# Kernel optimization log

Measured on AMD Instinct MI355X. Metric: run time of the kernel, lower is better.

The kernel has to match this reference:

```python
import jax, jax.numpy as jnp
import numpy as np

B, N, ATTR, H, OUT, STEPS = 8, 4096, 16, 64, 1, 8


def setup_inputs() -> dict:
    key = jax.random.key(0)
    ks = jax.random.split(key, 12)
    attr_matrix = jax.random.normal(ks[0], (B, N, ATTR), jnp.float32)
    adj_matrix = (jax.random.uniform(ks[1], (B, N, N)) < 0.01).astype(jnp.float32)
    s = float(1.0 / np.sqrt(H))
    u = lambda k, shape: jax.random.uniform(k, shape, jnp.float32, -s, s)
    Wi = jax.random.normal(ks[2], (H, ATTR), jnp.float32) * float(np.sqrt(2.0 / ATTR))  # kaiming
    bi = jnp.zeros((H,), jnp.float32)
    Wz = u(ks[3], (H, 3 * H)); bz = u(ks[4], (H,))
    Wr = u(ks[5], (H, 3 * H)); br = u(ks[6], (H,))
    Wh = u(ks[7], (H, 3 * H)); bh = u(ks[8], (H,))
    Wo = jax.random.normal(ks[9], (OUT, H), jnp.float32) * float(np.sqrt(2.0 / (H + OUT)))  # xavier
    bo = jnp.zeros((OUT,), jnp.float32)
    return dict(attr_matrix=attr_matrix, adj_matrix=adj_matrix, Wi=Wi, bi=bi,
                Wz=Wz, bz=bz, Wr=Wr, br=br, Wh=Wh, bh=bh, Wo=Wo, bo=bo)


def reference(attr_matrix, adj_matrix, Wi, bi, Wz, bz, Wr, br, Wh, bh, Wo, bo):
    # initial node states: (B, N, H)
    h = jax.nn.relu(attr_matrix @ Wi.T + bi)
    A_in = adj_matrix
    A_out = jnp.swapaxes(adj_matrix, -1, -2)
    for _ in range(STEPS):
        a_in = jnp.einsum('bij,bjh->bih', A_in, h)
        a_out = jnp.einsum('bij,bjh->bih', A_out, h)
        inp = jnp.concatenate([a_in, a_out], axis=-1)           # (B, N, 2H)
        xs = jnp.concatenate([inp, h], axis=-1)                  # (B, N, 3H)
        z = jax.nn.sigmoid(xs @ Wz.T + bz)
        r = jax.nn.sigmoid(xs @ Wr.T + br)
        hn = jnp.tanh(jnp.concatenate([inp, r * h], axis=-1) @ Wh.T + bh)
        h = (1.0 - z) * h + z * hn
    return h @ Wo.T + bo  # (B, N, OUT)
```

## Files before the change

kernel.cpp:

```cpp
#include <hip/hip_runtime.h>
#include <hip/hip_fp16.h>
#include <stdint.h>

#define BB 8
#define NN 4096
#define ATTRD 16
#define HD 64
#define STEPS 8
#define NODES (BB*NN)
#define ECAP 96
#define KPAD 196

typedef _Float16 half8 __attribute__((ext_vector_type(8)));
typedef float floatx4 __attribute__((ext_vector_type(4)));
typedef unsigned long long ull;

__global__ void init_h_kernel(const float* __restrict__ attr, const float* __restrict__ Wi,
                              const float* __restrict__ bi, float* __restrict__ h,
                              __half* __restrict__ h16) {
    int idx = blockIdx.x * blockDim.x + threadIdx.x;
    if (idx >= (NODES + 1) * HD) return;
    if (idx >= NODES * HD) {
        h16[idx] = __float2half(0.f);
        return;
    }
    int node = idx >> 6, l = idx & 63;
    const float* a = attr + node * ATTRD;
    const float* w = Wi + l * ATTRD;
    float acc = bi[l];
#pragma unroll
    for (int k = 0; k < ATTRD; k++) acc += a[k] * w[k];
    float r = acc > 0.f ? acc : 0.f;
    h[idx] = r;
    h16[idx] = __float2half(r);
}

__global__ void wprep_kernel(const float* __restrict__ Wz, const float* __restrict__ Wr,
                             const float* __restrict__ Wh,
                             _Float16* __restrict__ wf_hi, _Float16* __restrict__ wf_lo) {
    int t = blockIdx.x * blockDim.x + threadIdx.x;
    if (t >= 3 * 4 * 6 * 64 * 8) return;
    int mat = t / 12288, rem = t % 12288;
    int tile = rem / 3072, rem2 = rem % 3072;
    int kc = rem2 / 512, rem3 = rem2 % 512;
    int lane = rem3 / 8, j = rem3 % 8;
    int k = kc * 32 + (lane >> 4) * 8 + j;
    int och = tile * 16 + (lane & 15);
    const float* W = (mat == 0) ? Wz : (mat == 1) ? Wr : Wh;
    float v = W[och * 192 + k];
    _Float16 hi = (_Float16)v;
    wf_hi[t] = hi;
    wf_lo[t] = (_Float16)(v - (float)hi);
}

__global__ __launch_bounds__(256) void count_rows_kernel(const float4* __restrict__ A4,
                                                         int* __restrict__ cnt_in,
                                                         int* __restrict__ edge_in,
                                                         int* __restrict__ cnt_out,
                                                         int* __restrict__ edge_out) {
    int wave = threadIdx.x >> 6, l = threadIdx.x & 63;
    int row = blockIdx.x * 4 + wave;
    const float4* rp = A4 + (size_t)row * 1024;
    ull mask_lt = (l == 63) ? ~0ull >> 1 : ((1ull << (l + 1)) - 1) >> 1;
    float4 v[16];
#pragma unroll
    for (int t = 0; t < 16; t++) v[t] = rp[t * 64 + l];
    int colbase = (row >> 12) << 12;
    int run = 0;
    int* erow = edge_in + row * ECAP;
#pragma unroll
    for (int t = 0; t < 16; t++) {
        ull b0 = __ballot(v[t].x != 0.f);
        ull b1 = __ballot(v[t].y != 0.f);
        ull b2 = __ballot(v[t].z != 0.f);
        ull b3 = __ballot(v[t].w != 0.f);
        int pre = __popcll(b0 & mask_lt) + __popcll(b1 & mask_lt) +
                  __popcll(b2 & mask_lt) + __popcll(b3 & mask_lt);
        float vv[4] = {v[t].x, v[t].y, v[t].z, v[t].w};
        int jbase = (t * 64 + l) * 4;
        int inner = 0;
#pragma unroll
        for (int q = 0; q < 4; q++) {
            if (vv[q] != 0.f) {
                int col = colbase | (jbase + q);
                int slot = run + pre + inner;
                if (slot < ECAP) erow[slot] = col;
                inner++;
                int s2 = atomicAdd(&cnt_out[col], 1);
                if (s2 < ECAP) edge_out[col * ECAP + s2] = row;
            }
        }
        run += __popcll(b0) + __popcll(b1) + __popcll(b2) + __popcll(b3);
    }
    if (l == 0) cnt_in[row] = run;
}

__global__ __launch_bounds__(256) void aggregate_kernel(
        const uint4* __restrict__ h4, const float* __restrict__ h,
        const int* __restrict__ cnt_in, const int* __restrict__ edge_in,
        const int* __restrict__ cnt_out, const int* __restrict__ edge_out,
        float* __restrict__ xs) {
    int bid = blockIdx.x;
    int batch = bid & 7;
    int group = bid >> 3;
    int wave = threadIdx.x >> 6;
    int node = (batch << 12) + group * 4 + wave;
    int l = threadIdx.x & 63;
    int sub = l >> 3;
    int part = l & 7;
    int ni = cnt_in[node];  if (ni > ECAP) ni = ECAP;
    int no = cnt_out[node]; if (no > ECAP) no = ECAP;
    const int* ei = edge_in + node * ECAP;
    const int* eo = edge_out + node * ECAP;
    int ei0 = ei[l], ei1 = ei[64 + (l & 31)];
    int eo0 = eo[l], eo1 = eo[64 + (l & 31)];
    float ai[8] = {0.f, 0.f, 0.f, 0.f, 0.f, 0.f, 0.f, 0.f};
    float ao[8] = {0.f, 0.f, 0.f, 0.f, 0.f, 0.f, 0.f, 0.f};
    int nmax = ni > no ? ni : no;
    for (int s = 0; s < nmax; s += 32) {
        uint4 gA[4], gB[4];
#pragma unroll
        for (int k = 0; k < 4; k++) {
            int il = s + k * 8 + sub;
            int gi = (il < 64) ? __shfl(ei0, il) : __shfl(ei1, il - 64);
            int go = (il < 64) ? __shfl(eo0, il) : __shfl(eo1, il - 64);
            gi = (il < ni) ? gi : NODES;
            go = (il < no) ? go : NODES;
            gA[k] = h4[(gi << 3) | part];
            gB[k] = h4[(go << 3) | part];
        }
        const __half2* hA0 = (const __half2*)&gA[0];
        const __half2* hA1 = (const __half2*)&gA[1];
        const __half2* hA2 = (const __half2*)&gA[2];
        const __half2* hA3 = (const __half2*)&gA[3];
        const __half2* hB0 = (const __half2*)&gB[0];
        const __half2* hB1 = (const __half2*)&gB[1];
        const __half2* hB2 = (const __half2*)&gB[2];
        const __half2* hB3 = (const __half2*)&gB[3];
#pragma unroll
        for (int k = 0; k < 4; k++) {
            __half2 sA = __hadd2(__hadd2(hA0[k], hA1[k]), __hadd2(hA2[k], hA3[k]));
            __half2 sB = __hadd2(__hadd2(hB0[k], hB1[k]), __hadd2(hB2[k], hB3[k]));
            float2 fA = __half22float2(sA);
            float2 fB = __half22float2(sB);
            ai[2 * k] += fA.x; ai[2 * k + 1] += fA.y;
            ao[2 * k] += fB.x; ao[2 * k + 1] += fB.y;
        }
    }
#pragma unroll
    for (int off = 8; off < 64; off <<= 1) {
#pragma unroll
        for (int k = 0; k < 8; k++) {
            ai[k] += __shfl_xor(ai[k], off);
            ao[k] += __shfl_xor(ao[k], off);
        }
    }
    if (l < 8) {
        float* dst = xs + node * 192;
        float4 si0 = {ai[0], ai[1], ai[2], ai[3]};
        float4 si1 = {ai[4], ai[5], ai[6], ai[7]};
        float4 so0 = {ao[0], ao[1], ao[2], ao[3]};
        float4 so1 = {ao[4], ao[5], ao[6], ao[7]};
        *(float4*)(dst + l * 8)          = si0;
        *(float4*)(dst + l * 8 + 4)      = si1;
        *(float4*)(dst + 64 + l * 8)     = so0;
        *(float4*)(dst + 64 + l * 8 + 4) = so1;
    }
    xs[node * 192 + 128 + l] = h[(node << 6) | l];
}

__global__ __launch_bounds__(256) void gate_kernel(
        const float* __restrict__ xs_g,
        const _Float16* __restrict__ wf_hi, const _Float16* __restrict__ wf_lo,
        const float* __restrict__ bz, const float* __restrict__ br,
        const float* __restrict__ bh,
        float* __restrict__ h, __half* __restrict__ h16) {
    __shared__ float xs_t[16][KPAD];
    int bid = blockIdx.x;
    int base = ((bid & 7) << 12) | ((bid >> 3) << 4);
    int tid = threadIdx.x;
    {
        const float4* src = (const float4*)(xs_g + base * 192);
#pragma unroll
        for (int i = 0; i < 3; i++) {
            int idx = tid + i * 256;
            float4 v = src[idx];
            int nl = idx / 48, kb = (idx % 48) * 4;
            *(float4*)&xs_t[nl][kb] = v;
        }
    }
    __syncthreads();
    int wave = tid >> 6, lane = tid & 63;
    int m = lane & 15, q = lane >> 4;
    int ch = wave * 16 + m;
    const half8* WH = (const half8*)wf_hi;
    const half8* WL = (const half8*)wf_lo;

    floatx4 accz = {0.f, 0.f, 0.f, 0.f};
    floatx4 accr = {0.f, 0.f, 0.f, 0.f};
#pragma unroll
    for (int kc = 0; kc < 6; kc++) {
        const float* xr = &xs_t[m][kc * 32 + q * 8];
        float4 xa = *(const float4*)xr;
        float4 xb = *(const float4*)(xr + 4);
        float xv[8] = {xa.x, xa.y, xa.z, xa.w, xb.x, xb.y, xb.z, xb.w};
        half8 ahi, alo;
#pragma unroll
        for (int j = 0; j < 8; j++) {
            _Float16 hj = (_Float16)xv[j];
            ahi[j] = hj;
            alo[j] = (_Float16)(xv[j] - (float)hj);
        }
        half8 bzh = WH[((0 * 4 + wave) * 6 + kc) * 64 + lane];
        half8 bzl = WL[((0 * 4 + wave) * 6 + kc) * 64 + lane];
        half8 brh = WH[((1 * 4 + wave) * 6 + kc) * 64 + lane];
        half8 brl = WL[((1 * 4 + wave) * 6 + kc) * 64 + lane];
        accz = __builtin_amdgcn_mfma_f32_16x16x32_f16(ahi, bzh, accz, 0, 0, 0);
        accz = __builtin_amdgcn_mfma_f32_16x16x32_f16(alo, bzh, accz, 0, 0, 0);
        accz = __builtin_amdgcn_mfma_f32_16x16x32_f16(ahi, bzl, accz, 0, 0, 0);
        accr = __builtin_amdgcn_mfma_f32_16x16x32_f16(ahi, brh, accr, 0, 0, 0);
        accr = __builtin_amdgcn_mfma_f32_16x16x32_f16(alo, brh, accr, 0, 0, 0);
        accr = __builtin_amdgcn_mfma_f32_16x16x32_f16(ahi, brl, accr, 0, 0, 0);
    }
    float bzv = bz[ch], brv = br[ch], bhv = bh[ch];
    float zreg[4], hvreg[4], rh[4];
#pragma unroll
    for (int rg = 0; rg < 4; rg++) {
        int nl = q * 4 + rg;
        float z = 1.f / (1.f + __expf(-(accz[rg] + bzv)));
        float r = 1.f / (1.f + __expf(-(accr[rg] + brv)));
        float hv = xs_t[nl][128 + ch];
        zreg[rg] = z; hvreg[rg] = hv; rh[rg] = r * hv;
    }
    __syncthreads();
#pragma unroll
    for (int rg = 0; rg < 4; rg++) xs_t[q * 4 + rg][128 + ch] = rh[rg];
    __syncthreads();

    floatx4 acch = {0.f, 0.f, 0.f, 0.f};
#pragma unroll
    for (int kc = 0; kc < 6; kc++) {
        const float* xr = &xs_t[m][kc * 32 + q * 8];
        float4 xa = *(const float4*)xr;
        float4 xb = *(const float4*)(xr + 4);
        float xv[8] = {xa.x, xa.y, xa.z, xa.w, xb.x, xb.y, xb.z, xb.w};
        half8 ahi, alo;
#pragma unroll
        for (int j = 0; j < 8; j++) {
            _Float16 hj = (_Float16)xv[j];
            ahi[j] = hj;
            alo[j] = (_Float16)(xv[j] - (float)hj);
        }
        half8 bhh = WH[((2 * 4 + wave) * 6 + kc) * 64 + lane];
        half8 bhl = WL[((2 * 4 + wave) * 6 + kc) * 64 + lane];
        acch = __builtin_amdgcn_mfma_f32_16x16x32_f16(ahi, bhh, acch, 0, 0, 0);
        acch = __builtin_amdgcn_mfma_f32_16x16x32_f16(alo, bhh, acch, 0, 0, 0);
        acch = __builtin_amdgcn_mfma_f32_16x16x32_f16(ahi, bhl, acch, 0, 0, 0);
    }
    __syncthreads();
#pragma unroll
    for (int rg = 0; rg < 4; rg++) {
        int nl = q * 4 + rg;
        float pre = acch[rg] + bhv;
        float th = 2.f / (1.f + __expf(-2.f * pre)) - 1.f;
        float hv = hvreg[rg];
        xs_t[nl][ch] = hv + zreg[rg] * (th - hv);
    }
    __syncthreads();
    {
        int f = tid * 4;
        int nl = f >> 6, c = f & 63;
        float4 v = *(const float4*)&xs_t[nl][c];
        int gi = ((base + nl) << 6) | c;
        *(float4*)&h[gi] = v;
        __half2 p0 = {__float2half(v.x), __float2half(v.y)};
        __half2 p1 = {__float2half(v.z), __float2half(v.w)};
        *(__half2*)&h16[gi] = p0;
        *(__half2*)&h16[gi + 2] = p1;
    }
}

__global__ void out_kernel(const float* __restrict__ h, const float* __restrict__ Wo,
                           const float* __restrict__ bo, float* __restrict__ out) {
    int wid = (blockIdx.x * blockDim.x + threadIdx.x) >> 6;
    int l = threadIdx.x & 63;
    if (wid >= NODES) return;
    float p = h[(wid << 6) | l] * Wo[l];
#pragma unroll
    for (int off = 32; off > 0; off >>= 1) p += __shfl_down(p, off);
    if (l == 0) out[wid] = p + bo[0];
}

extern "C" void kernel_launch(void* const* d_in, const int* in_sizes, int n_in,
                              void* d_out, int out_size, void* d_ws, size_t ws_size,
                              hipStream_t stream) {
    const float* attr = (const float*)d_in[0];
    const float* adj  = (const float*)d_in[1];
    const float* Wi   = (const float*)d_in[2];
    const float* bi   = (const float*)d_in[3];
    const float* Wz   = (const float*)d_in[4];
    const float* bz   = (const float*)d_in[5];
    const float* Wr   = (const float*)d_in[6];
    const float* br   = (const float*)d_in[7];
    const float* Wh   = (const float*)d_in[8];
    const float* bh   = (const float*)d_in[9];
    const float* Wo   = (const float*)d_in[10];
    const float* bo   = (const float*)d_in[11];
    float* out = (float*)d_out;

    char* ws = (char*)d_ws;
    size_t off = 0;
    auto carve = [&](size_t bytes) { void* p = ws + off; off = (off + bytes + 255) & ~(size_t)255; return p; };
    float* h      = (float*)carve((size_t)NODES * HD * 4);
    __half* h16   = (__half*)carve((size_t)(NODES + 1) * HD * 2);
    float* xs     = (float*)carve((size_t)NODES * 192 * 4);
    _Float16* wf_hi = (_Float16*)carve(3 * 4 * 6 * 64 * 8 * 2);
    _Float16* wf_lo = (_Float16*)carve(3 * 4 * 6 * 64 * 8 * 2);
    int* cnt_in   = (int*)carve((size_t)NODES * 4);
    int* cnt_out  = (int*)carve((size_t)NODES * 4);
    int* edge_in  = (int*)carve((size_t)NODES * ECAP * 4);
    int* edge_out = (int*)carve((size_t)NODES * ECAP * 4);

    hipMemsetAsync(cnt_out, 0, (size_t)NODES * 4, stream);

    init_h_kernel<<<((NODES + 1) * HD + 255) / 256, 256, 0, stream>>>(attr, Wi, bi, h, h16);
    wprep_kernel<<<(3 * 4 * 6 * 64 * 8 + 255) / 256, 256, 0, stream>>>(Wz, Wr, Wh, wf_hi, wf_lo);
    count_rows_kernel<<<NODES / 4, 256, 0, stream>>>((const float4*)adj, cnt_in, edge_in,
                                                     cnt_out, edge_out);

    for (int step = 0; step < STEPS; ++step) {
        aggregate_kernel<<<NODES / 4, 256, 0, stream>>>(
            (const uint4*)h16, h, cnt_in, edge_in, cnt_out, edge_out, xs);
        gate_kernel<<<NODES / 16, 256, 0, stream>>>(xs, wf_hi, wf_lo, bz, br, bh, h, h16);
    }
    out_kernel<<<NODES * HD / 256, 256, 0, stream>>>(h, Wo, bo, out);
}
```

Baseline: 1.185 ms.

## Fuse aggregation and GRU gate into one step kernel with ping-pong h buffers

Merges the per-step aggregate and gate kernels into a single kernel that keeps the 192-wide concatenated input for 4 nodes in shared memory rather than writing and rereading an xs buffer in global memory. Because blocks now read neighbours' h while other blocks write the new state, h and its fp16 copy are double-buffered and swapped each step. The cost is that each block handles only 4 nodes, so the 16-row MFMA tiles are 3/4 redundant (rows are replicated via m&3), and weight loads are repeated by four times as many blocks.

```diff
diff --git a/kernel.cpp b/kernel.cpp
--- a/kernel.cpp
+++ b/kernel.cpp
@@ -17,11 +17,12 @@
 
 __global__ void init_h_kernel(const float* __restrict__ attr, const float* __restrict__ Wi,
                               const float* __restrict__ bi, float* __restrict__ h,
-                              __half* __restrict__ h16) {
+                              __half* __restrict__ h16a, __half* __restrict__ h16b) {
     int idx = blockIdx.x * blockDim.x + threadIdx.x;
     if (idx >= (NODES + 1) * HD) return;
     if (idx >= NODES * HD) {
-        h16[idx] = __float2half(0.f);
+        h16a[idx] = __float2half(0.f);
+        h16b[idx] = __float2half(0.f);
         return;
     }
     int node = idx >> 6, l = idx & 63;
@@ -32,7 +33,7 @@
     for (int k = 0; k < ATTRD; k++) acc += a[k] * w[k];
     float r = acc > 0.f ? acc : 0.f;
     h[idx] = r;
-    h16[idx] = __float2half(r);
+    h16a[idx] = __float2half(r);
 }
 
 __global__ void wprep_kernel(const float* __restrict__ Wz, const float* __restrict__ Wr,
@@ -95,17 +96,32 @@
     if (l == 0) cnt_in[row] = run;
 }
 
-__global__ __launch_bounds__(256) void aggregate_kernel(
-        const uint4* __restrict__ h4, const float* __restrict__ h,
+__global__ __launch_bounds__(256) void step_kernel(
+        const uint4* __restrict__ h4, const float* __restrict__ hg,
         const int* __restrict__ cnt_in, const int* __restrict__ edge_in,
         const int* __restrict__ cnt_out, const int* __restrict__ edge_out,
-        float* __restrict__ xs) {
+        const _Float16* __restrict__ wf_hi, const _Float16* __restrict__ wf_lo,
+        const float* __restrict__ bz, const float* __restrict__ br,
+        const float* __restrict__ bh,
+        float* __restrict__ h_out, __half* __restrict__ h16_out) {
+    __shared__ float xs_t[4][KPAD];
+    __shared__ float h32s[4][64];
+
     int bid = blockIdx.x;
     int batch = bid & 7;
     int group = bid >> 3;
-    int wave = threadIdx.x >> 6;
-    int node = (batch << 12) + group * 4 + wave;
-    int l = threadIdx.x & 63;
+    int node_base = (batch << 12) + group * 4;
+    int tid = threadIdx.x;
+    int wave = tid >> 6, l = tid & 63;
+
+    {
+        int nl = tid >> 6, c = tid & 63;
+        float v = hg[((node_base + nl) << 6) | c];
+        h32s[nl][c] = v;
+        xs_t[nl][128 + c] = v;
+    }
+
+    int node = node_base + wave;
     int sub = l >> 3;
     int part = l & 7;
     int ni = cnt_in[node];  if (ni > ECAP) ni = ECAP;
@@ -156,7 +172,7 @@
         }
     }
     if (l < 8) {
-        float* dst = xs + node * 192;
+        float* dst = &xs_t[wave][0];
         float4 si0 = {ai[0], ai[1], ai[2], ai[3]};
         float4 si1 = {ai[4], ai[5], ai[6], ai[7]};
         float4 so0 = {ao[0], ao[1], ao[2], ao[3]};
@@ -166,32 +182,10 @@
         *(float4*)(dst + 64 + l * 8)     = so0;
         *(float4*)(dst + 64 + l * 8 + 4) = so1;
     }
-    xs[node * 192 + 128 + l] = h[(node << 6) | l];
-}
-
-__global__ __launch_bounds__(256) void gate_kernel(
-        const float* __restrict__ xs_g,
-        const _Float16* __restrict__ wf_hi, const _Float16* __restrict__ wf_lo,
-        const float* __restrict__ bz, const float* __restrict__ br,
-        const float* __restrict__ bh,
-        float* __restrict__ h, __half* __restrict__ h16) {
-    __shared__ float xs_t[16][KPAD];
-    int bid = blockIdx.x;
-    int base = ((bid & 7) << 12) | ((bid >> 3) << 4);
-    int tid = threadIdx.x;
-    {
-        const float4* src = (const float4*)(xs_g + base * 192);
-#pragma unroll
-        for (int i = 0; i < 3; i++) {
-            int idx = tid + i * 256;
-            float4 v = src[idx];
-            int nl = idx / 48, kb = (idx % 48) * 4;
-            *(float4*)&xs_t[nl][kb] = v;
-        }
-    }
-    __syncthreads();
-    int wave = tid >> 6, lane = tid & 63;
-    int m = lane & 15, q = lane >> 4;
+    __syncthreads();
+
+    int m = l & 15, q = l >> 4;
+    int mm = m & 3;
     int ch = wave * 16 + m;
     const half8* WH = (const half8*)wf_hi;
     const half8* WL = (const half8*)wf_lo;
@@ -200,7 +194,7 @@
     floatx4 accr = {0.f, 0.f, 0.f, 0.f};
 #pragma unroll
     for (int kc = 0; kc < 6; kc++) {
-        const float* xr = &xs_t[m][kc * 32 + q * 8];
+        const float* xr = &xs_t[mm][kc * 32 + q * 8];
         float4 xa = *(const float4*)xr;
         float4 xb = *(const float4*)(xr + 4);
         float xv[8] = {xa.x, xa.y, xa.z, xa.w, xb.x, xb.y, xb.z, xb.w};
@@ -211,10 +205,10 @@
             ahi[j] = hj;
             alo[j] = (_Float16)(xv[j] - (float)hj);
         }
-        half8 bzh = WH[((0 * 4 + wave) * 6 + kc) * 64 + lane];
-        half8 bzl = WL[((0 * 4 + wave) * 6 + kc) * 64 + lane];
-        half8 brh = WH[((1 * 4 + wave) * 6 + kc) * 64 + lane];
-        half8 brl = WL[((1 * 4 + wave) * 6 + kc) * 64 + lane];
+        half8 bzh = WH[((0 * 4 + wave) * 6 + kc) * 64 + l];
+        half8 bzl = WL[((0 * 4 + wave) * 6 + kc) * 64 + l];
+        half8 brh = WH[((1 * 4 + wave) * 6 + kc) * 64 + l];
+        half8 brl = WL[((1 * 4 + wave) * 6 + kc) * 64 + l];
         accz = __builtin_amdgcn_mfma_f32_16x16x32_f16(ahi, bzh, accz, 0, 0, 0);
         accz = __builtin_amdgcn_mfma_f32_16x16x32_f16(alo, bzh, accz, 0, 0, 0);
         accz = __builtin_amdgcn_mfma_f32_16x16x32_f16(ahi, bzl, accz, 0, 0, 0);
@@ -226,21 +220,22 @@
     float zreg[4], hvreg[4], rh[4];
 #pragma unroll
     for (int rg = 0; rg < 4; rg++) {
-        int nl = q * 4 + rg;
         float z = 1.f / (1.f + __expf(-(accz[rg] + bzv)));
         float r = 1.f / (1.f + __expf(-(accr[rg] + brv)));
-        float hv = xs_t[nl][128 + ch];
+        float hv = h32s[rg & 3][ch];
         zreg[rg] = z; hvreg[rg] = hv; rh[rg] = r * hv;
     }
     __syncthreads();
-#pragma unroll
-    for (int rg = 0; rg < 4; rg++) xs_t[q * 4 + rg][128 + ch] = rh[rg];
+    if (q == 0) {
+#pragma unroll
+        for (int rg = 0; rg < 4; rg++) xs_t[rg][128 + ch] = rh[rg];
+    }
     __syncthreads();
 
     floatx4 acch = {0.f, 0.f, 0.f, 0.f};
 #pragma unroll
     for (int kc = 0; kc < 6; kc++) {
-        const float* xr = &xs_t[m][kc * 32 + q * 8];
+        const float* xr = &xs_t[mm][kc * 32 + q * 8];
         float4 xa = *(const float4*)xr;
         float4 xb = *(const float4*)(xr + 4);
         float xv[8] = {xa.x, xa.y, xa.z, xa.w, xb.x, xb.y, xb.z, xb.w};
@@ -251,32 +246,29 @@
             ahi[j] = hj;
             alo[j] = (_Float16)(xv[j] - (float)hj);
         }
-        half8 bhh = WH[((2 * 4 + wave) * 6 + kc) * 64 + lane];
-        half8 bhl = WL[((2 * 4 + wave) * 6 + kc) * 64 + lane];
+        half8 bhh = WH[((2 * 4 + wave) * 6 + kc) * 64 + l];
+        half8 bhl = WL[((2 * 4 + wave) * 6 + kc) * 64 + l];
         acch = __builtin_amdgcn_mfma_f32_16x16x32_f16(ahi, bhh, acch, 0, 0, 0);
         acch = __builtin_amdgcn_mfma_f32_16x16x32_f16(alo, bhh, acch, 0, 0, 0);
         acch = __builtin_amdgcn_mfma_f32_16x16x32_f16(ahi, bhl, acch, 0, 0, 0);
     }
     __syncthreads();
-#pragma unroll
-    for (int rg = 0; rg < 4; rg++) {
-        int nl = q * 4 + rg;
-        float pre = acch[rg] + bhv;
-        float th = 2.f / (1.f + __expf(-2.f * pre)) - 1.f;
-        float hv = hvreg[rg];
-        xs_t[nl][ch] = hv + zreg[rg] * (th - hv);
+    if (q == 0) {
+#pragma unroll
+        for (int rg = 0; rg < 4; rg++) {
+            float pre = acch[rg] + bhv;
+            float th = 2.f / (1.f + __expf(-2.f * pre)) - 1.f;
+            float hv = hvreg[rg];
+            xs_t[rg][ch] = hv + zreg[rg] * (th - hv);
+        }
     }
     __syncthreads();
     {
-        int f = tid * 4;
-        int nl = f >> 6, c = f & 63;
-        float4 v = *(const float4*)&xs_t[nl][c];
-        int gi = ((base + nl) << 6) | c;
-        *(float4*)&h[gi] = v;
-        __half2 p0 = {__float2half(v.x), __float2half(v.y)};
-        __half2 p1 = {__float2half(v.z), __float2half(v.w)};
-        *(__half2*)&h16[gi] = p0;
-        *(__half2*)&h16[gi + 2] = p1;
+        int nl = tid >> 6, c = tid & 63;
+        float v = xs_t[nl][c];
+        int gi = ((node_base + nl) << 6) | c;
+        h_out[gi] = v;
+        h16_out[gi] = __float2half(v);
     }
 }
 
@@ -311,9 +303,10 @@
     char* ws = (char*)d_ws;
     size_t off = 0;
     auto carve = [&](size_t bytes) { void* p = ws + off; off = (off + bytes + 255) & ~(size_t)255; return p; };
-    float* h      = (float*)carve((size_t)NODES * HD * 4);
-    __half* h16   = (__half*)carve((size_t)(NODES + 1) * HD * 2);
-    float* xs     = (float*)carve((size_t)NODES * 192 * 4);
+    float*  hA    = (float*)carve((size_t)NODES * HD * 4);
+    float*  hB    = (float*)carve((size_t)NODES * HD * 4);
+    __half* hA16  = (__half*)carve((size_t)(NODES + 1) * HD * 2);
+    __half* hB16  = (__half*)carve((size_t)(NODES + 1) * HD * 2);
     _Float16* wf_hi = (_Float16*)carve(3 * 4 * 6 * 64 * 8 * 2);
     _Float16* wf_lo = (_Float16*)carve(3 * 4 * 6 * 64 * 8 * 2);
     int* cnt_in   = (int*)carve((size_t)NODES * 4);
@@ -323,15 +316,19 @@
 
     hipMemsetAsync(cnt_out, 0, (size_t)NODES * 4, stream);
 
-    init_h_kernel<<<((NODES + 1) * HD + 255) / 256, 256, 0, stream>>>(attr, Wi, bi, h, h16);
+    init_h_kernel<<<((NODES + 1) * HD + 255) / 256, 256, 0, stream>>>(attr, Wi, bi, hA, hA16, hB16);
     wprep_kernel<<<(3 * 4 * 6 * 64 * 8 + 255) / 256, 256, 0, stream>>>(Wz, Wr, Wh, wf_hi, wf_lo);
     count_rows_kernel<<<NODES / 4, 256, 0, stream>>>((const float4*)adj, cnt_in, edge_in,
                                                      cnt_out, edge_out);
 
+    const float* hc = hA; const __half* hc16 = hA16;
+    float* hx = hB; __half* hx16 = hB16;
     for (int step = 0; step < STEPS; ++step) {
-        aggregate_kernel<<<NODES / 4, 256, 0, stream>>>(
-            (const uint4*)h16, h, cnt_in, edge_in, cnt_out, edge_out, xs);
-        gate_kernel<<<NODES / 16, 256, 0, stream>>>(xs, wf_hi, wf_lo, bz, br, bh, h, h16);
-    }
-    out_kernel<<<NODES * HD / 256, 256, 0, stream>>>(h, Wo, bo, out);
-}
+        step_kernel<<<NODES / 4, 256, 0, stream>>>(
+            (const uint4*)hc16, hc, cnt_in, edge_in, cnt_out, edge_out,
+            wf_hi, wf_lo, bz, br, bh, hx, hx16);
+        const float* tf = hc; hc = hx; hx = (float*)tf;
+        const __half* th = hc16; hc16 = hx16; hx16 = (__half*)th;
+    }
+    out_kernel<<<NODES * HD / 256, 256, 0, stream>>>(hc, Wo, bo, out);
+}
```

Result: slower. 1.391 ms (+17.4%).
